# Kernel optimization log

Measured on AMD Instinct MI355X. Metric: run time of the kernel, lower is better.

## Reference

```python
import jax, jax.numpy as jnp
import numpy as np

VOCAB, EMB, NB_CLASS = 100000, 50, 2
SEQ, BATCH = 512, 2048


def setup_inputs() -> dict:
    key = jax.random.key(0)
    ks = jax.random.split(key, 8)
    x = jax.random.randint(ks[0], (SEQ, BATCH), 0, VOCAB, dtype=jnp.int64 if jax.config.jax_enable_x64 else jnp.int32)
    x_lengths = jax.random.randint(ks[1], (BATCH,), 1, SEQ, dtype=jnp.int32)
    mask = jnp.ones((BATCH, SEQ), dtype=bool)
    emb_table = jax.random.normal(ks[2], (VOCAB, EMB), dtype=jnp.float32)
    s = 1.0 / np.sqrt(EMB)
    Wq = jax.random.uniform(ks[3], (EMB, EMB), jnp.float32, -s, s)
    bq = jax.random.uniform(ks[4], (EMB,), jnp.float32, -s, s)
    We = jax.random.uniform(ks[5], (EMB, EMB), jnp.float32, -s, s)
    be = jax.random.uniform(ks[6], (EMB,), jnp.float32, -s, s)
    Wo = jax.random.uniform(ks[7], (NB_CLASS, EMB), jnp.float32, -s, s)
    bo = jnp.zeros((NB_CLASS,), jnp.float32)
    return {"x": x, "x_lengths": x_lengths, "mask": mask,
            "emb_table": emb_table, "Wq": Wq, "bq": bq,
            "We": We, "be": be, "Wo": Wo, "bo": bo}


def reference(x, x_lengths, mask, emb_table, Wq, bq, We, be, Wo, bo):
    # embedded: [batch, seq, emb]
    embedded = jnp.transpose(emb_table[x], (1, 0, 2))
    mean_emb = jnp.mean(embedded, axis=1)                      # [B, E]
    q = mean_emb @ Wq.T + bq                                   # [B, E]
    scores = jnp.einsum('be,bse->bs', q, embedded)             # [B, S]
    scores = jnp.where(mask, scores, -jnp.inf)
    attention = jax.nn.softmax(scores, axis=1)                 # [B, S]
    emb_lin = embedded @ We.T + be                             # [B, S, E]
    pooled = jnp.einsum('bse,bs->be', emb_lin, attention)      # [B, E]
    yhat = pooled @ Wo.T + bo                                  # [B, nb_class]
    return yhat, attention
```

## Files before the change

### kernel.cpp

```cpp
#include <hip/hip_runtime.h>
#include <stdint.h>
#include <math.h>

constexpr int SEQ   = 512;
constexpr int BATCH = 2048;
constexpr int EMB   = 50;
constexpr int NBCLS = 2;
constexpr int VOCAB = 100000;
constexpr int NTHR  = 512;
constexpr int TPAD  = 32;
constexpr int LROW  = 25;

__device__ __forceinline__ uint32_t f32_to_bf16_rne(float f) {
    uint32_t u = __float_as_uint(f);
    return (u + 0x7fffu + ((u >> 16) & 1u)) >> 16;
}
__device__ __forceinline__ float bf16_lo(uint32_t u) { return __uint_as_float(u << 16); }
__device__ __forceinline__ float bf16_hi(uint32_t u) { return __uint_as_float(u & 0xffff0000u); }

constexpr int CONV_BLOCKS = VOCAB * TPAD / 256;
constexpr int TR_BLOCKS   = (SEQ / 32) * (BATCH / 32);

__global__ __launch_bounds__(256) void prologue(
    const float* __restrict__ t, uint32_t* __restrict__ o,
    const int* __restrict__ x, int* __restrict__ xT)
{
    __shared__ int tile[32][33];
    const int bid = blockIdx.x, tid = threadIdx.x;
    if (bid < CONV_BLOCKS) {
        int idx = bid * 256 + tid;
        int v = idx >> 5, c = idx & 31;
        uint32_t val = 0;
        if (c < 25) {
            float2 f = *reinterpret_cast<const float2*>(t + (long)v * EMB + 2 * c);
            val = f32_to_bf16_rne(f.x) | (f32_to_bf16_rne(f.y) << 16);
        }
        o[(long)v * TPAD + c] = val;
    } else {
        int b2 = bid - CONV_BLOCKS;
        int s0 = (b2 & 15) * 32, b0 = (b2 >> 4) * 32;
        int tx = tid & 31, ty = tid >> 5;
        #pragma unroll
        for (int j = 0; j < 32; j += 8) tile[ty + j][tx] = x[(s0 + ty + j) * BATCH + b0 + tx];
        __syncthreads();
        #pragma unroll
        for (int j = 0; j < 32; j += 8) xT[(b0 + ty + j) * SEQ + s0 + tx] = tile[tx][ty + j];
    }
}

__global__ __launch_bounds__(NTHR) void attn_main(
    const int*      __restrict__ xT,
    const uint32_t* __restrict__ tbl,
    const float* __restrict__ Wq, const float* __restrict__ bq,
    const float* __restrict__ We, const float* __restrict__ be,
    const float* __restrict__ Wo, const float* __restrict__ bo,
    float* __restrict__ out_yhat, float* __restrict__ out_att)
{
    const int b   = blockIdx.x;
    const int tid = threadIdx.x;

    __shared__ uint32_t embu[SEQ * LROW];
    __shared__ uint32_t attb[SEQ / 2];
    __shared__ float partials[8 * EMB];
    __shared__ float meanv[EMB];
    __shared__ float qv[EMB];
    __shared__ float red[8];

    {
        int t = xT[(long)b * SEQ + tid];
        const uint4* p = reinterpret_cast<const uint4*>(tbl + (long)t * TPAD);
        uint4 r[6];
        #pragma unroll
        for (int i = 0; i < 6; ++i) r[i] = p[i];
        uint32_t r6 = reinterpret_cast<const uint32_t*>(p)[24];
        uint32_t* dst = embu + tid * LROW;
        #pragma unroll
        for (int i = 0; i < 6; ++i) {
            dst[4 * i + 0] = r[i].x; dst[4 * i + 1] = r[i].y;
            dst[4 * i + 2] = r[i].z; dst[4 * i + 3] = r[i].w;
        }
        dst[24] = r6;
    }
    __syncthreads();

    if (tid < 200) {
        int c  = tid % 25;
        int ch = tid / 25;
        int s0 = ch * 64;
        float a0 = 0.f, a1 = 0.f;
        #pragma unroll 4
        for (int i = 0; i < 64; ++i) {
            int s = s0 + ((ch * 8 + i) & 63);
            uint32_t u = embu[s * LROW + c];
            a0 += bf16_lo(u); a1 += bf16_hi(u);
        }
        partials[ch * EMB + 2 * c]     = a0;
        partials[ch * EMB + 2 * c + 1] = a1;
    }
    __syncthreads();
    if (tid < EMB) {
        float acc = 0.f;
        #pragma unroll
        for (int ch = 0; ch < 8; ++ch) acc += partials[ch * EMB + tid];
        meanv[tid] = acc * (1.0f / SEQ);
    }
    __syncthreads();

    if (tid < EMB) {
        float acc = bq[tid];
        const float* wrow = Wq + tid * EMB;
        #pragma unroll 5
        for (int e = 0; e < EMB; ++e) acc += meanv[e] * wrow[e];
        qv[tid] = acc;
    }
    __syncthreads();

    float v;
    {
        const uint32_t* row = embu + tid * LROW;
        float acc = 0.f;
        #pragma unroll
        for (int c = 0; c < 25; ++c) {
            uint32_t u = row[c];
            acc += bf16_lo(u) * qv[2 * c] + bf16_hi(u) * qv[2 * c + 1];
        }
        v = acc;
    }

    const int lane = tid & 63;
    const int wave = tid >> 6;

    float m = v;
    #pragma unroll
    for (int off = 1; off < 64; off <<= 1) m = fmaxf(m, __shfl_xor(m, off));
    if (lane == 0) red[wave] = m;
    __syncthreads();
    if (tid == 0) {
        float mm = red[0];
        #pragma unroll
        for (int w = 1; w < 8; ++w) mm = fmaxf(mm, red[w]);
        red[0] = mm;
    }
    __syncthreads();
    const float maxv = red[0];
    const float ex = __expf(v - maxv);
    __syncthreads();

    float ssum = ex;
    #pragma unroll
    for (int off = 1; off < 64; off <<= 1) ssum += __shfl_xor(ssum, off);
    if (lane == 0) red[wave] = ssum;
    __syncthreads();
    if (tid == 0) {
        float t = 0.f;
        #pragma unroll
        for (int w = 0; w < 8; ++w) t += red[w];
        red[0] = 1.0f / t;
    }
    __syncthreads();
    const float att = ex * red[0];
    out_att[(long)b * SEQ + tid] = att;

    float attp = __shfl_xor(att, 1);
    if (!(tid & 1))
        attb[tid >> 1] = f32_to_bf16_rne(att) | (f32_to_bf16_rne(attp) << 16);
    __syncthreads();

    if (tid < 200) {
        int c  = tid % 25;
        int ch = tid / 25;
        int s0 = ch * 64;
        float a0 = 0.f, a1 = 0.f;
        #pragma unroll 4
        for (int i = 0; i < 64; ++i) {
            int s = s0 + ((ch * 8 + i) & 63);
            uint32_t u  = embu[s * LROW + c];
            uint32_t aw = attb[s >> 1];
            float a = __uint_as_float((s & 1) ? (aw & 0xffff0000u) : (aw << 16));
            a0 += a * bf16_lo(u); a1 += a * bf16_hi(u);
        }
        partials[ch * EMB + 2 * c]     = a0;
        partials[ch * EMB + 2 * c + 1] = a1;
    }
    __syncthreads();
    if (tid < EMB) {
        float acc = 0.f;
        #pragma unroll
        for (int ch = 0; ch < 8; ++ch) acc += partials[ch * EMB + tid];
        meanv[tid] = acc;
    }
    __syncthreads();

    if (tid < EMB) {
        float acc = be[tid];
        const float* wrow = We + tid * EMB;
        #pragma unroll 5
        for (int e = 0; e < EMB; ++e) acc += meanv[e] * wrow[e];
        qv[tid] = acc;
    }
    __syncthreads();
    if (tid < NBCLS) {
        float acc = bo[tid];
        const float* wrow = Wo + tid * EMB;
        #pragma unroll 5
        for (int e = 0; e < EMB; ++e) acc += qv[e] * wrow[e];
        out_yhat[(long)b * NBCLS + tid] = acc;
    }
}

__global__ __launch_bounds__(NTHR) void attn_fused_f32(
    const int*   __restrict__ x,
    const float* __restrict__ table,
    const float* __restrict__ Wq, const float* __restrict__ bq,
    const float* __restrict__ We, const float* __restrict__ be,
    const float* __restrict__ Wo, const float* __restrict__ bo,
    float* __restrict__ out_yhat, float* __restrict__ out_att)
{
    const int b   = blockIdx.x;
    const int tid = threadIdx.x;

    __shared__ float emb[SEQ * EMB];
    __shared__ int   toks[SEQ];
    __shared__ float scores[SEQ];
    __shared__ float red[8];
    __shared__ float partials[8 * EMB];
    __shared__ float meanv[EMB];
    __shared__ float qv[EMB];
    __shared__ float pooled[EMB];

    toks[tid] = x[tid * BATCH + b];
    __syncthreads();
    for (int idx = tid; idx < SEQ * (EMB / 2); idx += NTHR) {
        int s = idx / 25, e2 = idx - s * 25;
        long t = toks[s];
        float2 v = *reinterpret_cast<const float2*>(table + t * EMB + e2 * 2);
        *reinterpret_cast<float2*>(emb + s * EMB + e2 * 2) = v;
    }
    __syncthreads();
    if (tid < 8 * EMB) {
        int e = tid % EMB, c = tid / EMB, s0 = c * 64;
        float acc = 0.f;
        for (int i = 0; i < 64; ++i) acc += emb[(s0 + i) * EMB + e];
        partials[c * EMB + e] = acc;
    }
    __syncthreads();
    if (tid < EMB) {
        float acc = 0.f;
        for (int c = 0; c < 8; ++c) acc += partials[c * EMB + tid];
        meanv[tid] = acc * (1.0f / SEQ);
    }
    __syncthreads();
    if (tid < EMB) {
        float acc = bq[tid];
        const float* wrow = Wq + tid * EMB;
        for (int e = 0; e < EMB; ++e) acc += meanv[e] * wrow[e];
        qv[tid] = acc;
    }
    __syncthreads();
    {
        const float* row = emb + tid * EMB;
        float acc = 0.f;
        for (int e = 0; e < EMB; ++e) acc += qv[e] * row[e];
        scores[tid] = acc;
    }
    __syncthreads();
    const int lane = tid & 63, wave = tid >> 6;
    float v = scores[tid];
    float m = v;
    for (int off = 1; off < 64; off <<= 1) m = fmaxf(m, __shfl_xor(m, off));
    if (lane == 0) red[wave] = m;
    __syncthreads();
    if (tid == 0) {
        float mm = red[0];
        for (int w = 1; w < 8; ++w) mm = fmaxf(mm, red[w]);
        red[0] = mm;
    }
    __syncthreads();
    const float maxv = red[0];
    const float ex = __expf(v - maxv);
    __syncthreads();
    float ssum = ex;
    for (int off = 1; off < 64; off <<= 1) ssum += __shfl_xor(ssum, off);
    if (lane == 0) red[wave] = ssum;
    __syncthreads();
    if (tid == 0) {
        float t = 0.f;
        for (int w = 0; w < 8; ++w) t += red[w];
        red[0] = 1.0f / t;
    }
    __syncthreads();
    const float att = ex * red[0];
    scores[tid] = att;
    out_att[(long)b * SEQ + tid] = att;
    __syncthreads();
    if (tid < 8 * EMB) {
        int e = tid % EMB, c = tid / EMB, s0 = c * 64;
        float acc = 0.f;
        for (int i = 0; i < 64; ++i) acc += scores[s0 + i] * emb[(s0 + i) * EMB + e];
        partials[c * EMB + e] = acc;
    }
    __syncthreads();
    if (tid < EMB) {
        float acc = 0.f;
        for (int c = 0; c < 8; ++c) acc += partials[c * EMB + tid];
        pooled[tid] = acc;
    }
    __syncthreads();
    if (tid < EMB) {
        float acc = be[tid];
        const float* wrow = We + tid * EMB;
        for (int e = 0; e < EMB; ++e) acc += pooled[e] * wrow[e];
        qv[tid] = acc;
    }
    __syncthreads();
    if (tid < NBCLS) {
        float acc = bo[tid];
        const float* wrow = Wo + tid * EMB;
        for (int e = 0; e < EMB; ++e) acc += qv[e] * wrow[e];
        out_yhat[(long)b * NBCLS + tid] = acc;
    }
}

extern "C" void kernel_launch(void* const* d_in, const int* in_sizes, int n_in,
                              void* d_out, int out_size, void* d_ws, size_t ws_size,
                              hipStream_t stream) {
    const int*   x     = (const int*)  d_in[0];
    const float* table = (const float*)d_in[3];
    const float* Wq    = (const float*)d_in[4];
    const float* bq    = (const float*)d_in[5];
    const float* We    = (const float*)d_in[6];
    const float* be    = (const float*)d_in[7];
    const float* Wo    = (const float*)d_in[8];
    const float* bo    = (const float*)d_in[9];

    float* out_yhat = (float*)d_out;
    float* out_att  = (float*)d_out + (long)BATCH * NBCLS;

    const size_t tbl_bytes = (size_t)VOCAB * TPAD * 4;
    const size_t xt_bytes  = (size_t)BATCH * SEQ * 4;

    if (ws_size >= tbl_bytes + xt_bytes) {
        uint32_t* tbl16 = (uint32_t*)d_ws;
        int*      xT    = (int*)((char*)d_ws + tbl_bytes);
        prologue<<<CONV_BLOCKS + TR_BLOCKS, 256, 0, stream>>>(table, tbl16, x, xT);
        attn_main<<<BATCH, NTHR, 0, stream>>>(xT, tbl16, Wq, bq, We, be, Wo, bo,
                                              out_yhat, out_att);
    } else {
        attn_fused_f32<<<BATCH, NTHR, 0, stream>>>(x, table, Wq, bq, We, be, Wo, bo,
                                                   out_yhat, out_att);
    }
}
```

Baseline: 67.09 us.

## Keep embedding rows in registers and reduce via wave shuffles instead of LDS

The main kernel no longer stages the gathered bf16 embedding rows in a 51 KB shared buffer. Each thread keeps its 25 packed words in registers and computes the mean and attention-weighted sums with wave-wide xor-shuffle reductions per column. This removes the LDS footprint that limited blocks per CU and drops the strided LDS reduction passes, but it adds 50 shuffle chains per reduction and more register pressure under the new launch bound. The change also transposes Wq and We in the prologue so the matvec weight reads coalesce, and computes the output logits with a single-wave shuffle reduction.

```diff
diff --git a/kernel.cpp b/kernel.cpp
--- a/kernel.cpp
+++ b/kernel.cpp
@@ -9,7 +9,6 @@
 constexpr int VOCAB = 100000;
 constexpr int NTHR  = 512;
 constexpr int TPAD  = 32;
-constexpr int LROW  = 25;
 
 __device__ __forceinline__ uint32_t f32_to_bf16_rne(float f) {
     uint32_t u = __float_as_uint(f);
@@ -23,7 +22,9 @@
 
 __global__ __launch_bounds__(256) void prologue(
     const float* __restrict__ t, uint32_t* __restrict__ o,
-    const int* __restrict__ x, int* __restrict__ xT)
+    const int* __restrict__ x, int* __restrict__ xT,
+    const float* __restrict__ Wq, const float* __restrict__ We,
+    float* __restrict__ WqT, float* __restrict__ WeT)
 {
     __shared__ int tile[32][33];
     const int bid = blockIdx.x, tid = threadIdx.x;
@@ -36,7 +37,7 @@
             val = f32_to_bf16_rne(f.x) | (f32_to_bf16_rne(f.y) << 16);
         }
         o[(long)v * TPAD + c] = val;
-    } else {
+    } else if (bid < CONV_BLOCKS + TR_BLOCKS) {
         int b2 = bid - CONV_BLOCKS;
         int s0 = (b2 & 15) * 32, b0 = (b2 >> 4) * 32;
         int tx = tid & 31, ty = tid >> 5;
@@ -45,90 +46,80 @@
         __syncthreads();
         #pragma unroll
         for (int j = 0; j < 32; j += 8) xT[(b0 + ty + j) * SEQ + s0 + tx] = tile[tx][ty + j];
-    }
-}
-
-__global__ __launch_bounds__(NTHR) void attn_main(
+    } else {
+        for (int idx = tid; idx < EMB * EMB; idx += 256) {
+            int i = idx / EMB, j = idx - i * EMB;
+            WqT[j * EMB + i] = Wq[idx];
+            WeT[j * EMB + i] = We[idx];
+        }
+    }
+}
+
+__global__ __launch_bounds__(NTHR, 8) void attn_main(
     const int*      __restrict__ xT,
     const uint32_t* __restrict__ tbl,
-    const float* __restrict__ Wq, const float* __restrict__ bq,
-    const float* __restrict__ We, const float* __restrict__ be,
-    const float* __restrict__ Wo, const float* __restrict__ bo,
+    const float* __restrict__ WqT, const float* __restrict__ bq,
+    const float* __restrict__ WeT, const float* __restrict__ be,
+    const float* __restrict__ Wo,  const float* __restrict__ bo,
     float* __restrict__ out_yhat, float* __restrict__ out_att)
 {
-    const int b   = blockIdx.x;
-    const int tid = threadIdx.x;
-
-    __shared__ uint32_t embu[SEQ * LROW];
-    __shared__ uint32_t attb[SEQ / 2];
+    const int b    = blockIdx.x;
+    const int tid  = threadIdx.x;
+    const int lane = tid & 63;
+    const int wave = tid >> 6;
+
     __shared__ float partials[8 * EMB];
     __shared__ float meanv[EMB];
     __shared__ float qv[EMB];
     __shared__ float red[8];
 
+    uint32_t row[25];
     {
         int t = xT[(long)b * SEQ + tid];
         const uint4* p = reinterpret_cast<const uint4*>(tbl + (long)t * TPAD);
-        uint4 r[6];
-        #pragma unroll
-        for (int i = 0; i < 6; ++i) r[i] = p[i];
+        uint4 r0 = p[0], r1 = p[1], r2 = p[2], r3 = p[3], r4 = p[4], r5 = p[5];
         uint32_t r6 = reinterpret_cast<const uint32_t*>(p)[24];
-        uint32_t* dst = embu + tid * LROW;
-        #pragma unroll
-        for (int i = 0; i < 6; ++i) {
-            dst[4 * i + 0] = r[i].x; dst[4 * i + 1] = r[i].y;
-            dst[4 * i + 2] = r[i].z; dst[4 * i + 3] = r[i].w;
-        }
-        dst[24] = r6;
-    }
-    __syncthreads();
-
-    if (tid < 200) {
-        int c  = tid % 25;
-        int ch = tid / 25;
-        int s0 = ch * 64;
-        float a0 = 0.f, a1 = 0.f;
-        #pragma unroll 4
-        for (int i = 0; i < 64; ++i) {
-            int s = s0 + ((ch * 8 + i) & 63);
-            uint32_t u = embu[s * LROW + c];
-            a0 += bf16_lo(u); a1 += bf16_hi(u);
-        }
-        partials[ch * EMB + 2 * c]     = a0;
-        partials[ch * EMB + 2 * c + 1] = a1;
-    }
-    __syncthreads();
-    if (tid < EMB) {
-        float acc = 0.f;
-        #pragma unroll
-        for (int ch = 0; ch < 8; ++ch) acc += partials[ch * EMB + tid];
+        row[0]=r0.x; row[1]=r0.y; row[2]=r0.z; row[3]=r0.w;
+        row[4]=r1.x; row[5]=r1.y; row[6]=r1.z; row[7]=r1.w;
+        row[8]=r2.x; row[9]=r2.y; row[10]=r2.z; row[11]=r2.w;
+        row[12]=r3.x; row[13]=r3.y; row[14]=r3.z; row[15]=r3.w;
+        row[16]=r4.x; row[17]=r4.y; row[18]=r4.z; row[19]=r4.w;
+        row[20]=r5.x; row[21]=r5.y; row[22]=r5.z; row[23]=r5.w;
+        row[24]=r6;
+    }
+
+    #pragma unroll
+    for (int c = 0; c < 25; ++c) {
+        float lo = bf16_lo(row[c]), hi = bf16_hi(row[c]);
+        #pragma unroll
+        for (int m = 1; m < 64; m <<= 1) {
+            lo += __shfl_xor(lo, m);
+            hi += __shfl_xor(hi, m);
+        }
+        if (lane == c)
+            *reinterpret_cast<float2*>(&partials[wave * EMB + 2 * c]) = make_float2(lo, hi);
+    }
+    __syncthreads();
+    if (tid < EMB) {
+        float acc = 0.f;
+        #pragma unroll
+        for (int w = 0; w < 8; ++w) acc += partials[w * EMB + tid];
         meanv[tid] = acc * (1.0f / SEQ);
     }
     __syncthreads();
 
     if (tid < EMB) {
         float acc = bq[tid];
-        const float* wrow = Wq + tid * EMB;
         #pragma unroll 5
-        for (int e = 0; e < EMB; ++e) acc += meanv[e] * wrow[e];
+        for (int e = 0; e < EMB; ++e) acc += meanv[e] * WqT[e * EMB + tid];
         qv[tid] = acc;
     }
     __syncthreads();
 
-    float v;
-    {
-        const uint32_t* row = embu + tid * LROW;
-        float acc = 0.f;
-        #pragma unroll
-        for (int c = 0; c < 25; ++c) {
-            uint32_t u = row[c];
-            acc += bf16_lo(u) * qv[2 * c] + bf16_hi(u) * qv[2 * c + 1];
-        }
-        v = acc;
-    }
-
-    const int lane = tid & 63;
-    const int wave = tid >> 6;
+    float v = 0.f;
+    #pragma unroll
+    for (int c = 0; c < 25; ++c)
+        v += bf16_lo(row[c]) * qv[2 * c] + bf16_hi(row[c]) * qv[2 * c + 1];
 
     float m = v;
     #pragma unroll
@@ -161,50 +152,47 @@
     const float att = ex * red[0];
     out_att[(long)b * SEQ + tid] = att;
 
-    float attp = __shfl_xor(att, 1);
-    if (!(tid & 1))
-        attb[tid >> 1] = f32_to_bf16_rne(att) | (f32_to_bf16_rne(attp) << 16);
-    __syncthreads();
-
-    if (tid < 200) {
-        int c  = tid % 25;
-        int ch = tid / 25;
-        int s0 = ch * 64;
-        float a0 = 0.f, a1 = 0.f;
-        #pragma unroll 4
-        for (int i = 0; i < 64; ++i) {
-            int s = s0 + ((ch * 8 + i) & 63);
-            uint32_t u  = embu[s * LROW + c];
-            uint32_t aw = attb[s >> 1];
-            float a = __uint_as_float((s & 1) ? (aw & 0xffff0000u) : (aw << 16));
-            a0 += a * bf16_lo(u); a1 += a * bf16_hi(u);
-        }
-        partials[ch * EMB + 2 * c]     = a0;
-        partials[ch * EMB + 2 * c + 1] = a1;
-    }
-    __syncthreads();
-    if (tid < EMB) {
-        float acc = 0.f;
-        #pragma unroll
-        for (int ch = 0; ch < 8; ++ch) acc += partials[ch * EMB + tid];
+    #pragma unroll
+    for (int c = 0; c < 25; ++c) {
+        float lo = att * bf16_lo(row[c]), hi = att * bf16_hi(row[c]);
+        #pragma unroll
+        for (int m2 = 1; m2 < 64; m2 <<= 1) {
+            lo += __shfl_xor(lo, m2);
+            hi += __shfl_xor(hi, m2);
+        }
+        if (lane == c)
+            *reinterpret_cast<float2*>(&partials[wave * EMB + 2 * c]) = make_float2(lo, hi);
+    }
+    __syncthreads();
+    if (tid < EMB) {
+        float acc = 0.f;
+        #pragma unroll
+        for (int w = 0; w < 8; ++w) acc += partials[w * EMB + tid];
         meanv[tid] = acc;
     }
     __syncthreads();
 
     if (tid < EMB) {
         float acc = be[tid];
-        const float* wrow = We + tid * EMB;
         #pragma unroll 5
-        for (int e = 0; e < EMB; ++e) acc += meanv[e] * wrow[e];
+        for (int e = 0; e < EMB; ++e) acc += meanv[e] * WeT[e * EMB + tid];
         qv[tid] = acc;
     }
     __syncthreads();
-    if (tid < NBCLS) {
-        float acc = bo[tid];
-        const float* wrow = Wo + tid * EMB;
-        #pragma unroll 5
-        for (int e = 0; e < EMB; ++e) acc += qv[e] * wrow[e];
-        out_yhat[(long)b * NBCLS + tid] = acc;
+
+    if (wave == 0) {
+        float pv = (lane < EMB) ? qv[lane] : 0.f;
+        float a0 = (lane < EMB) ? pv * Wo[lane]       : 0.f;
+        float a1 = (lane < EMB) ? pv * Wo[EMB + lane] : 0.f;
+        #pragma unroll
+        for (int off = 1; off < 64; off <<= 1) {
+            a0 += __shfl_xor(a0, off);
+            a1 += __shfl_xor(a1, off);
+        }
+        if (lane == 0) {
+            out_yhat[(long)b * NBCLS + 0] = a0 + bo[0];
+            out_yhat[(long)b * NBCLS + 1] = a1 + bo[1];
+        }
     }
 }
 
@@ -258,9 +246,9 @@
     }
     __syncthreads();
     {
-        const float* row = emb + tid * EMB;
-        float acc = 0.f;
-        for (int e = 0; e < EMB; ++e) acc += qv[e] * row[e];
+        const float* rowp = emb + tid * EMB;
+        float acc = 0.f;
+        for (int e = 0; e < EMB; ++e) acc += qv[e] * rowp[e];
         scores[tid] = acc;
     }
     __syncthreads();
@@ -338,12 +326,16 @@
 
     const size_t tbl_bytes = (size_t)VOCAB * TPAD * 4;
     const size_t xt_bytes  = (size_t)BATCH * SEQ * 4;
-
-    if (ws_size >= tbl_bytes + xt_bytes) {
+    const size_t w_bytes   = (size_t)EMB * EMB * 4;
+
+    if (ws_size >= tbl_bytes + xt_bytes + 2 * w_bytes) {
         uint32_t* tbl16 = (uint32_t*)d_ws;
         int*      xT    = (int*)((char*)d_ws + tbl_bytes);
-        prologue<<<CONV_BLOCKS + TR_BLOCKS, 256, 0, stream>>>(table, tbl16, x, xT);
-        attn_main<<<BATCH, NTHR, 0, stream>>>(xT, tbl16, Wq, bq, We, be, Wo, bo,
+        float*    WqT   = (float*)((char*)d_ws + tbl_bytes + xt_bytes);
+        float*    WeT   = (float*)((char*)d_ws + tbl_bytes + xt_bytes + w_bytes);
+        prologue<<<CONV_BLOCKS + TR_BLOCKS + 1, 256, 0, stream>>>(
+            table, tbl16, x, xT, Wq, We, WqT, WeT);
+        attn_main<<<BATCH, NTHR, 0, stream>>>(xT, tbl16, WqT, bq, WeT, be, Wo, bo,
                                               out_yhat, out_att);
     } else {
         attn_fused_f32<<<BATCH, NTHR, 0, stream>>>(x, table, Wq, bq, We, be, Wo, bo,
```

Measured after the change: 144.2 us. 115% more time.
